# Optimization experiments

Measured on AMD Instinct MI355X. Metric: run time of the kernel, lower is better.

## Reference

```python
import jax, jax.numpy as jnp
import numpy as np

NUM_GROUPS = 32
EPS = 1e-6


def group_norm(x, scale, bias):
    b, c, h, w = x.shape
    g = NUM_GROUPS
    xg = x.reshape(b, g, c // g, h, w)
    mean = jnp.mean(xg, axis=(2, 3, 4), keepdims=True)
    var = jnp.var(xg, axis=(2, 3, 4), keepdims=True)
    xg = (xg - mean) * jax.lax.rsqrt(var + EPS)
    x = xg.reshape(b, c, h, w)
    return x * scale[None, :, None, None] + bias[None, :, None, None]


def conv1x1(x, w, b):
    # x: [B,C,H,W], w: [Cout,Cin], b: [Cout]
    return jnp.einsum('bchw,oc->bohw', x, w) + b[None, :, None, None]


def setup_inputs() -> dict:
    key = jax.random.key(0)
    ks = jax.random.split(key, 11)
    C = 512
    B, H, W = 8, 64, 64
    s = 1.0 / np.sqrt(C)
    inp = {
        'x': jax.random.normal(ks[0], (B, C, H, W), jnp.float32),
        'gn_scale': jnp.ones((C,), jnp.float32),
        'gn_bias': jnp.zeros((C,), jnp.float32),
        'wq': jax.random.normal(ks[1], (C, C), jnp.float32) * s,
        'bq': jnp.zeros((C,), jnp.float32),
        'wk': jax.random.normal(ks[2], (C, C), jnp.float32) * s,
        'bk': jnp.zeros((C,), jnp.float32),
        'wv': jax.random.normal(ks[3], (C, C), jnp.float32) * s,
        'bv': jnp.zeros((C,), jnp.float32),
    }
    return inp


def reference(x, gn_scale, gn_bias, wq, bq, wk, bk, wv, bv):
    b, c, h, w = x.shape
    h_ = group_norm(x, gn_scale, gn_bias)
    q = conv1x1(h_, wq, bq).reshape(b, c, h * w)  # [b,c,n]
    k = conv1x1(h_, wk, bk).reshape(b, c, h * w)
    v = conv1x1(h_, wv, bv).reshape(b, c, h * w)
    scale = jnp.asarray(c, x.dtype) ** -0.5
    # attn[b,i,j] = sum_c q[b,c,i] * k[b,c,j]
    attn = jnp.einsum('bci,bcj->bij', q, k) * scale
    attn = jax.nn.softmax(attn, axis=2)  # softmax over j (keys)
    # A[b,c,i] = sum_j v[b,c,j] * attn[b,i,j]
    A = jnp.einsum('bcj,bij->bci', v, attn).reshape(b, c, h, w)
    return x + A
```

## Files before the change

kernel.cpp:

```cpp
#include <hip/hip_runtime.h>
#include <hip/hip_bf16.h>

#define B_   8
#define C_   512
#define N_   4096
#define G_   32
#define CPG  16
#define EPSV 1e-6f

typedef short s16x8 __attribute__((ext_vector_type(8)));
typedef float f32x4 __attribute__((ext_vector_type(4)));

__device__ __forceinline__ unsigned short f2bf(float f) {
    unsigned u = __builtin_bit_cast(unsigned, f);
    u += 0x7fffu + ((u >> 16) & 1u);
    return (unsigned short)(u >> 16);
}

__device__ __forceinline__ void gload_lds16(const unsigned short* g, unsigned short* l) {
    __builtin_amdgcn_global_load_lds((const __attribute__((address_space(1))) void*)g,
                                     (__attribute__((address_space(3))) void*)l, 16, 0, 0);
}

__global__ __launch_bounds__(256) void gn_stats_k(const float* __restrict__ x,
                                                  float* __restrict__ stats) {
    int blk = blockIdx.x;
    const float4* p = (const float4*)(x + (size_t)blk * (CPG * N_));
    float s = 0.f, ss = 0.f;
    for (int i = threadIdx.x; i < (CPG * N_) / 4; i += 256) {
        float4 v = p[i];
        s  += v.x + v.y + v.z + v.w;
        ss += v.x * v.x + v.y * v.y + v.z * v.z + v.w * v.w;
    }
    for (int off = 32; off > 0; off >>= 1) {
        s  += __shfl_down(s, off);
        ss += __shfl_down(ss, off);
    }
    __shared__ float r0[4], r1[4];
    int wid = threadIdx.x >> 6;
    if ((threadIdx.x & 63) == 0) { r0[wid] = s; r1[wid] = ss; }
    __syncthreads();
    if (threadIdx.x == 0) {
        s  = r0[0] + r0[1] + r0[2] + r0[3];
        ss = r1[0] + r1[1] + r1[2] + r1[3];
        const float inv = 1.0f / (CPG * N_);
        float mean = s * inv;
        float var  = ss * inv - mean * mean;
        stats[2 * blk]     = mean;
        stats[2 * blk + 1] = rsqrtf(var + EPSV);
    }
}

__global__ __launch_bounds__(256) void cvt_w_k(const float* __restrict__ wq,
                                               const float* __restrict__ wk,
                                               const float* __restrict__ wv,
                                               unsigned short* __restrict__ wbf) {
    int i = blockIdx.x * 256 + threadIdx.x;
    const int percc = C_ * C_ / 4;
    const float* src; int li;
    if (i < percc)            { src = wq; li = i; }
    else if (i < 2 * percc)   { src = wk; li = i - percc; }
    else                      { src = wv; li = i - 2 * percc; }
    float4 v = ((const float4*)src)[li];
    unsigned u0 = (unsigned)f2bf(v.x) | ((unsigned)f2bf(v.y) << 16);
    unsigned u1 = (unsigned)f2bf(v.z) | ((unsigned)f2bf(v.w) << 16);
    uint2 o; o.x = u0; o.y = u1;
    *(uint2*)&wbf[(size_t)i * 4] = o;
}

__global__ __launch_bounds__(256) void gn_apply_k(const float* __restrict__ x,
                                                  const float* __restrict__ stats,
                                                  const float* __restrict__ gsc,
                                                  const float* __restrict__ gbi,
                                                  unsigned short* __restrict__ h_t) {
    int nt = blockIdx.x, ct = blockIdx.y, b = blockIdx.z;
    int n0 = nt * 64, c0 = ct * 64;
    __shared__ unsigned short T[64][72];
    int t = threadIdx.x;
    int cl = t >> 2, ch = t & 3;
    int c = c0 + cl;
    int g = c >> 4;
    float mean = stats[(b * G_ + g) * 2];
    float rstd = stats[(b * G_ + g) * 2 + 1];
    float sc = gsc[c] * rstd;
    float bi = gbi[c] - mean * sc;
    const float* xr = x + (size_t)(b * C_ + c) * N_ + n0 + ch * 16;
    #pragma unroll
    for (int q = 0; q < 4; ++q) {
        float4 v = *(const float4*)(xr + q * 4);
        int nl = ch * 16 + q * 4;
        T[nl + 0][cl] = f2bf(fmaf(v.x, sc, bi));
        T[nl + 1][cl] = f2bf(fmaf(v.y, sc, bi));
        T[nl + 2][cl] = f2bf(fmaf(v.z, sc, bi));
        T[nl + 3][cl] = f2bf(fmaf(v.w, sc, bi));
    }
    __syncthreads();
    #pragma unroll
    for (int it = 0; it < 2; ++it) {
        int id = t + it * 256;
        int nl = id >> 3, part = id & 7;
        s16x8 val = *(const s16x8*)&T[nl][part * 8];
        *(s16x8*)&h_t[((size_t)b * N_ + n0 + nl) * C_ + c0 + part * 8] = val;
    }
}

__global__ __launch_bounds__(256) void copyx_k(const float* __restrict__ x,
                                               float* __restrict__ out) {
    const size_t total4 = (size_t)B_ * C_ * N_ / 4;
    size_t stride = (size_t)gridDim.x * 256;
    for (size_t i = blockIdx.x * 256 + threadIdx.x; i < total4; i += stride)
        ((float4*)out)[i] = ((const float4*)x)[i];
}

__device__ __forceinline__ void gemm_core(const unsigned short* A, int ldA,
                                          const unsigned short* Bm, int ldB,
                                          unsigned short* Al, unsigned short* Bl,
                                          f32x4 (&acc)[4][4], int ksteps, int t) {
    int w = t >> 6, l = t & 63;
    int wm = (w >> 1) * 64, wn = (w & 1) * 64;
    int lr = l & 15, lg = l >> 4;
    int srow = w * 16 + (l >> 2);
    int sp   = (l & 3) * 8;

    #pragma unroll
    for (int it = 0; it < 2; ++it) {
        gload_lds16(&A [(size_t)(it * 64 + srow) * ldA + sp], &Al[it * 2048 + w * 512 + l * 8]);
        gload_lds16(&Bm[(size_t)(it * 64 + srow) * ldB + sp], &Bl[it * 2048 + w * 512 + l * 8]);
    }
    __syncthreads();

    int cur = 0;
    for (int s = 0; s < ksteps; ++s) {
        if (s + 1 < ksteps) {
            const unsigned short* ga = A  + (s + 1) * 32;
            const unsigned short* gb = Bm + (s + 1) * 32;
            int off = (cur ^ 1) * 4096;
            #pragma unroll
            for (int it = 0; it < 2; ++it) {
                gload_lds16(&ga[(size_t)(it * 64 + srow) * ldA + sp], &Al[off + it * 2048 + w * 512 + l * 8]);
                gload_lds16(&gb[(size_t)(it * 64 + srow) * ldB + sp], &Bl[off + it * 2048 + w * 512 + l * 8]);
            }
        }
        const unsigned short* la = Al + cur * 4096;
        const unsigned short* lb = Bl + cur * 4096;
        s16x8 a[4], b[4];
        #pragma unroll
        for (int i = 0; i < 4; ++i) a[i] = *(const s16x8*)&la[(wm + i * 16 + lr) * 32 + lg * 8];
        #pragma unroll
        for (int j = 0; j < 4; ++j) b[j] = *(const s16x8*)&lb[(wn + j * 16 + lr) * 32 + lg * 8];
        #pragma unroll
        for (int i = 0; i < 4; ++i)
            #pragma unroll
            for (int j = 0; j < 4; ++j)
                acc[i][j] = __builtin_amdgcn_mfma_f32_16x16x32_bf16(a[i], b[j], acc[i][j], 0, 0, 0);
        __syncthreads();
        cur ^= 1;
    }
}

__global__ __launch_bounds__(256, 4) void qkv_k(const unsigned short* __restrict__ h_t,
                                                const unsigned short* __restrict__ wbf,
                                                const float* __restrict__ bq,
                                                const float* __restrict__ bk,
                                                const float* __restrict__ bv,
                                                unsigned short* __restrict__ q_t,
                                                unsigned short* __restrict__ k_t,
                                                unsigned short* __restrict__ vv) {
    int which = blockIdx.z % 3;
    int b     = blockIdx.z / 3;
    int bx = blockIdx.x, by = blockIdx.y;
    const unsigned short* A;
    const unsigned short* Bm;
    unsigned short* Cm;
    const float* bias;
    int m0, n0; size_t ldc; bool biasRow;
    const unsigned short* hb = h_t + (size_t)b * N_ * C_;
    if (which < 2) {
        A = hb; Bm = wbf + (size_t)which * C_ * C_;
        Cm = (which == 0 ? q_t : k_t) + (size_t)b * N_ * C_;
        bias = (which == 0 ? bq : bk);
        m0 = bx * 128; n0 = by * 128; ldc = C_; biasRow = false;
    } else {
        A = wbf + (size_t)2 * C_ * C_; Bm = hb;
        Cm = vv + (size_t)b * C_ * N_;
        bias = bv;
        m0 = by * 128; n0 = bx * 128; ldc = N_; biasRow = true;
    }

    __shared__ char smem[35072];
    unsigned short* Al = (unsigned short*)smem;
    unsigned short* Bl = Al + 8192;
    unsigned short* El = (unsigned short*)smem;

    int t = threadIdx.x;
    int wid = t >> 6, lane = t & 63;
    int wm = (wid >> 1) * 64, wn = (wid & 1) * 64;
    int lr = lane & 15, lg = lane >> 4;

    f32x4 acc[4][4] = {};
    gemm_core(A + (size_t)m0 * C_, C_, Bm + (size_t)n0 * C_, C_, Al, Bl, acc, C_ / 32, t);

    float rb[4][4], cb[4];
    #pragma unroll
    for (int i = 0; i < 4; ++i)
        #pragma unroll
        for (int r = 0; r < 4; ++r)
            rb[i][r] = biasRow ? bias[m0 + wm + i * 16 + lg * 4 + r] : 0.f;
    #pragma unroll
    for (int j = 0; j < 4; ++j)
        cb[j] = biasRow ? 0.f : bias[n0 + wn + j * 16 + lr];

    #pragma unroll
    for (int i = 0; i < 4; ++i)
        #pragma unroll
        for (int j = 0; j < 4; ++j) {
            int col = wn + j * 16 + lr;
            #pragma unroll
            for (int r = 0; r < 4; ++r) {
                int row = wm + i * 16 + lg * 4 + r;
                El[row * 136 + col] = f2bf(acc[i][j][r] + rb[i][r] + cb[j]);
            }
        }
    __syncthreads();
    #pragma unroll
    for (int it = 0; it < 8; ++it) {
        int id = t + it * 256;
        int row = id >> 4, part = id & 15;
        *(s16x8*)&Cm[(size_t)(m0 + row) * ldc + n0 + part * 8] =
            *(const s16x8*)&El[row * 136 + part * 8];
    }
}

__global__ __launch_bounds__(512) void zeroL_k(float* __restrict__ L) {
    L[blockIdx.x * 512 + threadIdx.x] = 0.f;
}

__global__ __launch_bounds__(256, 4) void sgemm_k(const unsigned short* __restrict__ q_t,
                                                  const unsigned short* __restrict__ k_t,
                                                  unsigned short* __restrict__ Ptil,
                                                  float* __restrict__ L,
                                                  int bbase) {
    int z = blockIdx.z;
    int b = bbase + z;
    const unsigned short* A  = q_t + (size_t)b * N_ * C_;
    const unsigned short* Bm = k_t + (size_t)b * N_ * C_;
    unsigned short* Cm = Ptil + (size_t)z * N_ * N_;
    int m0 = blockIdx.y * 128, n0 = blockIdx.x * 128;

    __shared__ char smem[35072];
    unsigned short* Al = (unsigned short*)smem;
    unsigned short* Bl = Al + 8192;
    unsigned short* El = (unsigned short*)smem;

    int t = threadIdx.x;
    int wid = t >> 6, lane = t & 63;
    int wm = (wid >> 1) * 64, wn = (wid & 1) * 64;
    int lr = lane & 15, lg = lane >> 4;

    f32x4 acc[4][4] = {};
    gemm_core(A + (size_t)m0 * C_, C_, Bm + (size_t)n0 * C_, C_, Al, Bl, acc, C_ / 32, t);

    const float SCL2 = 0.06375862f;
    float rsum[4][4];
    #pragma unroll
    for (int i = 0; i < 4; ++i)
        #pragma unroll
        for (int r = 0; r < 4; ++r) rsum[i][r] = 0.f;

    #pragma unroll
    for (int i = 0; i < 4; ++i)
        #pragma unroll
        for (int j = 0; j < 4; ++j) {
            int col = wn + j * 16 + lr;
            #pragma unroll
            for (int r = 0; r < 4; ++r) {
                float p = exp2f(acc[i][j][r] * SCL2);
                rsum[i][r] += p;
                El[(wm + i * 16 + lg * 4 + r) * 136 + col] = f2bf(p);
            }
        }
    #pragma unroll
    for (int msk = 8; msk >= 1; msk >>= 1)
        #pragma unroll
        for (int i = 0; i < 4; ++i)
            #pragma unroll
            for (int r = 0; r < 4; ++r)
                rsum[i][r] += __shfl_xor(rsum[i][r], msk);
    if (lr == 0) {
        #pragma unroll
        for (int i = 0; i < 4; ++i)
            #pragma unroll
            for (int r = 0; r < 4; ++r)
                atomicAdd(&L[(size_t)b * N_ + m0 + wm + i * 16 + lg * 4 + r], rsum[i][r]);
    }
    __syncthreads();
    #pragma unroll
    for (int it = 0; it < 8; ++it) {
        int id = t + it * 256;
        int row = id >> 4, part = id & 15;
        *(s16x8*)&Cm[(size_t)(m0 + row) * N_ + n0 + part * 8] =
            *(const s16x8*)&El[row * 136 + part * 8];
    }
}

template <bool ATOMIC>
__global__ __launch_bounds__(256, 4) void pv_k(const unsigned short* __restrict__ vv,
                                               const unsigned short* __restrict__ Ptil,
                                               const float* __restrict__ L,
                                               const float* __restrict__ x,
                                               float* __restrict__ out,
                                               int bbase, int SK) {
    int z = blockIdx.z;
    int slot = z / SK, kr = z % SK;
    int b = bbase + slot;
    int kOff = kr * (N_ / SK);
    const unsigned short* A  = vv + (size_t)b * C_ * N_ + kOff;
    const unsigned short* Bm = Ptil + (size_t)slot * N_ * N_ + kOff;
    int m0 = blockIdx.y * 128, n0 = blockIdx.x * 128;
    const float* xb = x + (size_t)b * C_ * N_;
    float* ob = out + (size_t)b * C_ * N_;

    __shared__ char smem[32768];
    unsigned short* Al = (unsigned short*)smem;
    unsigned short* Bl = Al + 8192;

    int t = threadIdx.x;
    int wid = t >> 6, lane = t & 63;
    int wm = (wid >> 1) * 64, wn = (wid & 1) * 64;
    int lr = lane & 15, lg = lane >> 4;

    f32x4 acc[4][4] = {};
    gemm_core(A + (size_t)m0 * N_, N_, Bm + (size_t)n0 * N_, N_, Al, Bl, acc, (N_ / SK) / 32, t);

    #pragma unroll
    for (int j = 0; j < 4; ++j) {
        int col = n0 + wn + j * 16 + lr;
        float rl = 1.0f / L[(size_t)b * N_ + col];
        #pragma unroll
        for (int i = 0; i < 4; ++i) {
            #pragma unroll
            for (int r = 0; r < 4; ++r) {
                int row = m0 + wm + i * 16 + lg * 4 + r;
                size_t off = (size_t)row * N_ + col;
                if (ATOMIC) atomicAdd(&ob[off], acc[i][j][r] * rl);
                else        ob[off] = xb[off] + acc[i][j][r] * rl;
            }
        }
    }
}

extern "C" void kernel_launch(void* const* d_in, const int* in_sizes, int n_in,
                              void* d_out, int out_size, void* d_ws, size_t ws_size,
                              hipStream_t stream) {
    const float* x   = (const float*)d_in[0];
    const float* gsc = (const float*)d_in[1];
    const float* gbi = (const float*)d_in[2];
    const float* wq  = (const float*)d_in[3];
    const float* bq  = (const float*)d_in[4];
    const float* wk  = (const float*)d_in[5];
    const float* bk  = (const float*)d_in[6];
    const float* wv  = (const float*)d_in[7];
    const float* bv  = (const float*)d_in[8];
    float* out = (float*)d_out;

    const size_t elems = (size_t)B_ * N_ * C_;
    unsigned short* q_t   = (unsigned short*)d_ws;
    unsigned short* k_t   = q_t + elems;
    unsigned short* v     = k_t + elems;
    float*          stats = (float*)(v + elems);
    unsigned short* wbf   = (unsigned short*)(stats + 2 * B_ * G_);
    float*          L     = (float*)(wbf + (size_t)3 * C_ * C_);
    unsigned short* Ptil  = (unsigned short*)(L + (size_t)B_ * N_);
    unsigned short* h_t   = (unsigned short*)d_out;

    const size_t base_bytes = (size_t)((char*)Ptil - (char*)d_ws);
    const size_t slot_bytes = (size_t)N_ * N_ * 2;
    int slots = 2;
    if      (ws_size >= base_bytes + 8 * slot_bytes) slots = 8;
    else if (ws_size >= base_bytes + 4 * slot_bytes) slots = 4;
    const int SK = 8 / slots;

    gn_stats_k<<<B_ * G_, 256, 0, stream>>>(x, stats);
    cvt_w_k<<<(3 * C_ * C_ / 4) / 256, 256, 0, stream>>>(wq, wk, wv, wbf);
    gn_apply_k<<<dim3(N_ / 64, C_ / 64, B_), 256, 0, stream>>>(x, stats, gsc, gbi, h_t);
    qkv_k<<<dim3(32, 4, 3 * B_), 256, 0, stream>>>(h_t, wbf, bq, bk, bv, q_t, k_t, v);
    zeroL_k<<<(B_ * N_) / 512, 512, 0, stream>>>(L);

    if (slots == 8) {
        sgemm_k<<<dim3(32, 32, 8), 256, 0, stream>>>(q_t, k_t, Ptil, L, 0);
        pv_k<false><<<dim3(32, 4, 8), 256, 0, stream>>>(v, Ptil, L, x, out, 0, 1);
    } else {
        copyx_k<<<2048, 256, 0, stream>>>(x, out);
        for (int bb = 0; bb < B_; bb += slots) {
            sgemm_k<<<dim3(32, 32, slots), 256, 0, stream>>>(q_t, k_t, Ptil, L, bb);
            pv_k<true><<<dim3(32, 4, 8), 256, 0, stream>>>(v, Ptil, L, x, out, bb, SK);
        }
    }
}
```

Before: 624.4 us.

## Use 256x256 tiles with 512-thread blocks for score and PV GEMMs

Replaces the 128x128 score and PV GEMM kernels with 256x256-tile versions that use 512 threads, 8x4 MFMA accumulators per wave, and double-buffered LDS staging. The larger tiles raise arithmetic intensity and cut redundant global loads of Q/K and V/P. PV now always uses split-K with atomic accumulation into an output pre-filled with x, using more splits so the grid stays large enough. The cost is much more LDS per block (128 KB), lower occupancy, and more atomic traffic to the output.

Result: slower. 904.5 us (+44.8%).

```diff
diff --git a/kernel.cpp b/kernel.cpp
--- a/kernel.cpp
+++ b/kernel.cpp
@@ -235,40 +235,89 @@
     L[blockIdx.x * 512 + threadIdx.x] = 0.f;
 }
 
-__global__ __launch_bounds__(256, 4) void sgemm_k(const unsigned short* __restrict__ q_t,
+__device__ __forceinline__ void stage256b(const unsigned short* g, int ldg,
+                                          unsigned short* dst, int tid) {
+    int r0 = tid >> 2, c = tid & 3;
+    #pragma unroll
+    for (int i = 0; i < 2; ++i) {
+        int row = r0 + i * 128;
+        int cs = c ^ (row & 3);
+        gload_lds16(&g[(size_t)row * ldg + cs * 8], &dst[row * 32 + c * 8]);
+    }
+}
+
+__device__ __forceinline__ void gemm256_core(const unsigned short* A, int ldA,
+                                             const unsigned short* Bm, int ldB,
+                                             unsigned short* sm, int nt,
+                                             f32x4 (&acc)[8][4]) {
+    const int tid = threadIdx.x;
+    const int w = tid >> 6, l = tid & 63;
+    const int lr = l & 15, lg = l >> 4;
+    const int wm = (w >> 2) * 128, wn = (w & 3) * 64;
+    unsigned short* Asm = sm;
+    unsigned short* Bsm = sm + 2 * 8192;
+
+    stage256b(A, ldA, Asm, tid);
+    stage256b(Bm, ldB, Bsm, tid);
+    __syncthreads();
+
+    for (int t = 0; t < nt; ++t) {
+        const int cur = (t & 1) * 8192;
+        if (t + 1 < nt) {
+            const int nxt = ((t + 1) & 1) * 8192;
+            stage256b(A  + (size_t)(t + 1) * 32, ldA, Asm + nxt, tid);
+            stage256b(Bm + (size_t)(t + 1) * 32, ldB, Bsm + nxt, tid);
+        }
+        s16x8 av[8], bv[4];
+        #pragma unroll
+        for (int i = 0; i < 8; ++i) {
+            int row = wm + i * 16 + lr;
+            av[i] = *(const s16x8*)&Asm[cur + row * 32 + ((lg ^ (row & 3)) * 8)];
+        }
+        #pragma unroll
+        for (int j = 0; j < 4; ++j) {
+            int row = wn + j * 16 + lr;
+            bv[j] = *(const s16x8*)&Bsm[cur + row * 32 + ((lg ^ (row & 3)) * 8)];
+        }
+        #pragma unroll
+        for (int i = 0; i < 8; ++i)
+            #pragma unroll
+            for (int j = 0; j < 4; ++j)
+                acc[i][j] = __builtin_amdgcn_mfma_f32_16x16x32_bf16(av[i], bv[j], acc[i][j], 0, 0, 0);
+        __syncthreads();
+    }
+}
+
+__global__ __launch_bounds__(512) void sgemm256_k(const unsigned short* __restrict__ q_t,
                                                   const unsigned short* __restrict__ k_t,
                                                   unsigned short* __restrict__ Ptil,
                                                   float* __restrict__ L,
                                                   int bbase) {
+    __shared__ char smem[131072];
     int z = blockIdx.z;
     int b = bbase + z;
-    const unsigned short* A  = q_t + (size_t)b * N_ * C_;
-    const unsigned short* Bm = k_t + (size_t)b * N_ * C_;
-    unsigned short* Cm = Ptil + (size_t)z * N_ * N_;
-    int m0 = blockIdx.y * 128, n0 = blockIdx.x * 128;
-
-    __shared__ char smem[35072];
-    unsigned short* Al = (unsigned short*)smem;
-    unsigned short* Bl = Al + 8192;
+    int m0 = blockIdx.y * 256, n0 = blockIdx.x * 256;
+    const unsigned short* A  = q_t + (size_t)b * N_ * C_ + (size_t)m0 * C_;
+    const unsigned short* Bm = k_t + (size_t)b * N_ * C_ + (size_t)n0 * C_;
+
+    f32x4 acc[8][4] = {};
+    gemm256_core(A, C_, Bm, C_, (unsigned short*)smem, C_ / 32, acc);
+
+    const int tid = threadIdx.x;
+    const int w = tid >> 6, l = tid & 63;
+    const int lr = l & 15, lg = l >> 4;
+    const int wm = (w >> 2) * 128, wn = (w & 3) * 64;
+    const float SCL2 = 0.06375862f;
+
     unsigned short* El = (unsigned short*)smem;
-
-    int t = threadIdx.x;
-    int wid = t >> 6, lane = t & 63;
-    int wm = (wid >> 1) * 64, wn = (wid & 1) * 64;
-    int lr = lane & 15, lg = lane >> 4;
-
-    f32x4 acc[4][4] = {};
-    gemm_core(A + (size_t)m0 * C_, C_, Bm + (size_t)n0 * C_, C_, Al, Bl, acc, C_ / 32, t);
-
-    const float SCL2 = 0.06375862f;
-    float rsum[4][4];
-    #pragma unroll
-    for (int i = 0; i < 4; ++i)
+    float rsum[8][4];
+    #pragma unroll
+    for (int i = 0; i < 8; ++i)
         #pragma unroll
         for (int r = 0; r < 4; ++r) rsum[i][r] = 0.f;
 
     #pragma unroll
-    for (int i = 0; i < 4; ++i)
+    for (int i = 0; i < 8; ++i)
         #pragma unroll
         for (int j = 0; j < 4; ++j) {
             int col = wn + j * 16 + lr;
@@ -276,74 +325,67 @@
             for (int r = 0; r < 4; ++r) {
                 float p = exp2f(acc[i][j][r] * SCL2);
                 rsum[i][r] += p;
-                El[(wm + i * 16 + lg * 4 + r) * 136 + col] = f2bf(p);
+                El[(wm + i * 16 + lg * 4 + r) * 256 + col] = f2bf(p);
             }
         }
     #pragma unroll
     for (int msk = 8; msk >= 1; msk >>= 1)
         #pragma unroll
-        for (int i = 0; i < 4; ++i)
+        for (int i = 0; i < 8; ++i)
             #pragma unroll
             for (int r = 0; r < 4; ++r)
                 rsum[i][r] += __shfl_xor(rsum[i][r], msk);
     if (lr == 0) {
         #pragma unroll
-        for (int i = 0; i < 4; ++i)
+        for (int i = 0; i < 8; ++i)
             #pragma unroll
             for (int r = 0; r < 4; ++r)
                 atomicAdd(&L[(size_t)b * N_ + m0 + wm + i * 16 + lg * 4 + r], rsum[i][r]);
     }
     __syncthreads();
-    #pragma unroll
-    for (int it = 0; it < 8; ++it) {
-        int id = t + it * 256;
-        int row = id >> 4, part = id & 15;
+    unsigned short* Cm = Ptil + (size_t)z * N_ * N_;
+    #pragma unroll
+    for (int it = 0; it < 16; ++it) {
+        int u = tid + it * 512;
+        int row = u >> 5, part = u & 31;
         *(s16x8*)&Cm[(size_t)(m0 + row) * N_ + n0 + part * 8] =
-            *(const s16x8*)&El[row * 136 + part * 8];
-    }
-}
-
-template <bool ATOMIC>
-__global__ __launch_bounds__(256, 4) void pv_k(const unsigned short* __restrict__ vv,
+            *(const s16x8*)&El[row * 256 + part * 8];
+    }
+}
+
+__global__ __launch_bounds__(512) void pv256_k(const unsigned short* __restrict__ vv,
                                                const unsigned short* __restrict__ Ptil,
                                                const float* __restrict__ L,
-                                               const float* __restrict__ x,
                                                float* __restrict__ out,
                                                int bbase, int SK) {
+    __shared__ char smem[65536];
     int z = blockIdx.z;
     int slot = z / SK, kr = z % SK;
     int b = bbase + slot;
     int kOff = kr * (N_ / SK);
-    const unsigned short* A  = vv + (size_t)b * C_ * N_ + kOff;
-    const unsigned short* Bm = Ptil + (size_t)slot * N_ * N_ + kOff;
-    int m0 = blockIdx.y * 128, n0 = blockIdx.x * 128;
-    const float* xb = x + (size_t)b * C_ * N_;
+    int m0 = blockIdx.y * 256, n0 = blockIdx.x * 256;
+    const unsigned short* A  = vv   + (size_t)b * C_ * N_ + (size_t)m0 * N_ + kOff;
+    const unsigned short* Bm = Ptil + (size_t)slot * N_ * N_ + (size_t)n0 * N_ + kOff;
     float* ob = out + (size_t)b * C_ * N_;
 
-    __shared__ char smem[32768];
-    unsigned short* Al = (unsigned short*)smem;
-    unsigned short* Bl = Al + 8192;
-
-    int t = threadIdx.x;
-    int wid = t >> 6, lane = t & 63;
-    int wm = (wid >> 1) * 64, wn = (wid & 1) * 64;
-    int lr = lane & 15, lg = lane >> 4;
-
-    f32x4 acc[4][4] = {};
-    gemm_core(A + (size_t)m0 * N_, N_, Bm + (size_t)n0 * N_, N_, Al, Bl, acc, (N_ / SK) / 32, t);
+    f32x4 acc[8][4] = {};
+    gemm256_core(A, N_, Bm, N_, (unsigned short*)smem, (N_ / SK) / 32, acc);
+
+    const int tid = threadIdx.x;
+    const int w = tid >> 6, l = tid & 63;
+    const int lr = l & 15, lg = l >> 4;
+    const int wm = (w >> 2) * 128, wn = (w & 3) * 64;
 
     #pragma unroll
     for (int j = 0; j < 4; ++j) {
         int col = n0 + wn + j * 16 + lr;
         float rl = 1.0f / L[(size_t)b * N_ + col];
         #pragma unroll
-        for (int i = 0; i < 4; ++i) {
+        for (int i = 0; i < 8; ++i) {
             #pragma unroll
             for (int r = 0; r < 4; ++r) {
                 int row = m0 + wm + i * 16 + lg * 4 + r;
-                size_t off = (size_t)row * N_ + col;
-                if (ATOMIC) atomicAdd(&ob[off], acc[i][j][r] * rl);
-                else        ob[off] = xb[off] + acc[i][j][r] * rl;
+                atomicAdd(&ob[(size_t)row * N_ + col], acc[i][j][r] * rl);
             }
         }
     }
@@ -378,22 +420,17 @@
     int slots = 2;
     if      (ws_size >= base_bytes + 8 * slot_bytes) slots = 8;
     else if (ws_size >= base_bytes + 4 * slot_bytes) slots = 4;
-    const int SK = 8 / slots;
+    const int SK = 32 / slots;
 
     gn_stats_k<<<B_ * G_, 256, 0, stream>>>(x, stats);
     cvt_w_k<<<(3 * C_ * C_ / 4) / 256, 256, 0, stream>>>(wq, wk, wv, wbf);
     gn_apply_k<<<dim3(N_ / 64, C_ / 64, B_), 256, 0, stream>>>(x, stats, gsc, gbi, h_t);
     qkv_k<<<dim3(32, 4, 3 * B_), 256, 0, stream>>>(h_t, wbf, bq, bk, bv, q_t, k_t, v);
     zeroL_k<<<(B_ * N_) / 512, 512, 0, stream>>>(L);
-
-    if (slots == 8) {
-        sgemm_k<<<dim3(32, 32, 8), 256, 0, stream>>>(q_t, k_t, Ptil, L, 0);
-        pv_k<false><<<dim3(32, 4, 8), 256, 0, stream>>>(v, Ptil, L, x, out, 0, 1);
-    } else {
-        copyx_k<<<2048, 256, 0, stream>>>(x, out);
-        for (int bb = 0; bb < B_; bb += slots) {
-            sgemm_k<<<dim3(32, 32, slots), 256, 0, stream>>>(q_t, k_t, Ptil, L, bb);
-            pv_k<true><<<dim3(32, 4, 8), 256, 0, stream>>>(v, Ptil, L, x, out, bb, SK);
-        }
-    }
-}
+    copyx_k<<<2048, 256, 0, stream>>>(x, out);
+
+    for (int bb = 0; bb < B_; bb += slots) {
+        sgemm256_k<<<dim3(16, 16, slots), 512, 0, stream>>>(q_t, k_t, Ptil, L, bb);
+        pv256_k<<<dim3(16, 2, 32), 512, 0, stream>>>(v, Ptil, L, out, bb, SK);
+    }
+}
```
